# Optimization experiments

Measured on AMD Instinct MI355X. Metric: run time of the kernel, lower is better.

Reference implementation:

```python
import jax, jax.numpy as jnp
import numpy as np

N, M, DIM_K, DIM_V = 8192, 8192, 256, 256

def setup_inputs() -> dict:
    key = jax.random.key(0)
    kq, kk, kv = jax.random.split(key, 3)
    Q = jax.random.normal(kq, (N, DIM_K), dtype=jnp.float32)
    K = jax.random.normal(kk, (M, DIM_K), dtype=jnp.float32)
    V = jax.random.normal(kv, (M, DIM_V), dtype=jnp.float32)
    return {"Q": Q, "K": K, "V": V}

def reference(Q, K, V):
    # scores: [N, M] = Q @ K^T / sqrt(dim_k)
    scale = 1.0 / jnp.sqrt(jnp.asarray(Q.shape[-1], dtype=Q.dtype))
    scores = jnp.einsum('nd,md->nm', Q, K) * scale
    attn = jax.nn.softmax(scores, axis=-1)  # softmax over keys
    return attn @ V  # [N, dim_v]
```

## Files before the change

### kernel.cpp

```cpp
#include <hip/hip_runtime.h>
#include <hip/hip_bf16.h>


typedef __attribute__((ext_vector_type(16))) float floatx16;
typedef __attribute__((ext_vector_type(8)))  short short8;

union S8u { short8 v; unsigned short u[8]; };

__device__ __forceinline__ unsigned short f2bf(float f) {
    unsigned int u = __builtin_bit_cast(unsigned int, f);
    unsigned int r = u + 0x7fffu + ((u >> 16) & 1u);
    return (unsigned short)(r >> 16);
}

__device__ __forceinline__ unsigned cvtpk_bf16(float lo, float hi) {
    unsigned r;
    asm("v_cvt_pk_bf16_f32 %0, %1, %2" : "=v"(r) : "v"(lo), "v"(hi));
    return r;
}

__device__ __forceinline__ void gload16(const void* g, void* l) {
    __builtin_amdgcn_global_load_lds(
        (const __attribute__((address_space(1))) unsigned int*)g,
        (__attribute__((address_space(3))) unsigned int*)l, 16, 0, 0);
}


__global__ void cvt_bf16_kernel(const float* __restrict__ in,
                                unsigned short* __restrict__ out,
                                float scale, int n8) {
    int i = blockIdx.x * blockDim.x + threadIdx.x;
    if (i >= n8) return;
    const float4* p = reinterpret_cast<const float4*>(in) + (size_t)i * 2;
    float4 a = p[0], b = p[1];
    S8u r;
    r.u[0] = f2bf(a.x * scale); r.u[1] = f2bf(a.y * scale);
    r.u[2] = f2bf(a.z * scale); r.u[3] = f2bf(a.w * scale);
    r.u[4] = f2bf(b.x * scale); r.u[5] = f2bf(b.y * scale);
    r.u[6] = f2bf(b.z * scale); r.u[7] = f2bf(b.w * scale);
    *reinterpret_cast<short8*>(out + (size_t)i * 8) = r.v;
}

__global__ void transpose_v_kernel(const float* __restrict__ V,
                                   unsigned short* __restrict__ Vt) {
    __shared__ unsigned short T[64][72];
    const int kv0 = blockIdx.x * 64;
    const int v0  = blockIdx.y * 64;
    const int tid = threadIdx.x;
#pragma unroll
    for (int it = 0; it < 4; ++it) {
        int flat = it * 256 + tid;
        int r  = flat >> 4;
        int c4 = (flat & 15) * 4;
        float4 f = *reinterpret_cast<const float4*>(
            V + (size_t)(kv0 + r) * 256 + v0 + c4);
        T[c4 + 0][r] = f2bf(f.x);
        T[c4 + 1][r] = f2bf(f.y);
        T[c4 + 2][r] = f2bf(f.z);
        T[c4 + 3][r] = f2bf(f.w);
    }
    __syncthreads();
#pragma unroll
    for (int it = 0; it < 2; ++it) {
        int flat = it * 256 + tid;
        int r  = flat >> 3;
        int c8 = (flat & 7) * 8;
        short8 v8 = *reinterpret_cast<const short8*>(&T[r][c8]);
        *reinterpret_cast<short8*>(Vt + (size_t)(v0 + r) * 8192 + kv0 + c8) = v8;
    }
}


__global__ __launch_bounds__(512, 2)
void attn_kernel(const unsigned short* __restrict__ Qb,
                 const unsigned short* __restrict__ Kb,
                 const unsigned short* __restrict__ VtG,
                 float* __restrict__ Opart,
                 float* __restrict__ Ml,
                 int kv_span, int gshift) {
    __shared__ __align__(16) unsigned char lds[2][65536];

    const int tid  = threadIdx.x;
    const int lane = tid & 63;
    const int w    = tid >> 6;
    const int l31  = lane & 31;
    const int h    = lane >> 5;

    const int ngm1 = (1 << gshift) - 1;
    const int id   = blockIdx.x + 32 * blockIdx.y;
    const int g    = id & ngm1;
    const int qblk = id >> gshift;
    const int kv_begin = g * kv_span;
    const int tiles = kv_span >> 6;
    const int q0 = qblk * 256 + w * 32;

    short8 qf[16];
    {
        const unsigned short* qp = Qb + (size_t)(q0 + l31) * 256 + h * 8;
#pragma unroll
        for (int ds = 0; ds < 16; ++ds)
            qf[ds] = *reinterpret_cast<const short8*>(qp + ds * 16);
    }

    floatx16 o[8];
#pragma unroll
    for (int vt = 0; vt < 8; ++vt)
#pragma unroll
        for (int r = 0; r < 16; ++r) o[vt][r] = 0.f;
    float m_run = -1e30f, l_run = 0.f;

    auto STAGE = [&](int kv0, int bufsel) {
        unsigned char* kb = &lds[bufsel][0];
        unsigned char* vb = &lds[bufsel][32768];
#pragma unroll
        for (int i = 0; i < 4; ++i) {
            int j = w * 4 + i;
            {
                int row = j * 2 + (lane >> 5);
                int c   = lane & 31;
                int cs  = c ^ (row & 7);
                gload16(Kb + (size_t)(kv0 + row) * 256 + cs * 8, kb + j * 1024);
            }
            {
                int row = j * 8 + (lane >> 3);
                int c   = lane & 7;
                int cs  = c ^ (row & 7);
                gload16(VtG + (size_t)row * 8192 + kv0 + cs * 8, vb + j * 1024);
            }
        }
    };

    STAGE(kv_begin, 0);
    asm volatile("s_waitcnt vmcnt(0)" ::: "memory");
    __syncthreads();

    const int swz = l31 & 7;

    for (int t = 0; t < tiles; ++t) {
        const int cur = t & 1;
        if (t + 1 < tiles) STAGE(kv_begin + (t + 1) * 64, cur ^ 1);

        const unsigned char* kl = &lds[cur][0];
        const unsigned char* vl = &lds[cur][32768];

        floatx16 s0, s1;
#pragma unroll
        for (int r = 0; r < 16; ++r) { s0[r] = 0.f; s1[r] = 0.f; }
#pragma unroll
        for (int ds = 0; ds < 16; ++ds) {
            int c0 = (ds * 2 + h) ^ swz;
            short8 a0 = *reinterpret_cast<const short8*>(kl + (size_t)l31 * 512 + c0 * 16);
            short8 a1 = *reinterpret_cast<const short8*>(kl + (size_t)(l31 + 32) * 512 + c0 * 16);
            s0 = __builtin_amdgcn_mfma_f32_32x32x16_bf16(a0, qf[ds], s0, 0, 0, 0);
            s1 = __builtin_amdgcn_mfma_f32_32x32x16_bf16(a1, qf[ds], s1, 0, 0, 0);
        }

        float mt = s0[0];
#pragma unroll
        for (int r = 1; r < 16; ++r) mt = fmaxf(mt, s0[r]);
#pragma unroll
        for (int r = 0; r < 16; ++r) mt = fmaxf(mt, s1[r]);
        mt = fmaxf(mt, __shfl_xor(mt, 32));
        if (__any(mt > m_run + 8.0f)) {
            float mnew = fmaxf(m_run, mt);
            float al = __expf(m_run - mnew);
            m_run = mnew;
            l_run *= al;
#pragma unroll
            for (int reg = 0; reg < 16; ++reg) {
                int srcl = ((reg & 3) + 8 * (reg >> 2)) + 4 * h;
                float alr = __shfl(al, srcl);
#pragma unroll
                for (int vt = 0; vt < 8; ++vt) o[vt][reg] *= alr;
            }
        }
        float lt = 0.f;
#pragma unroll
        for (int r = 0; r < 16; ++r) { float p = __expf(s0[r] - m_run); s0[r] = p; lt += p; }
#pragma unroll
        for (int r = 0; r < 16; ++r) { float p = __expf(s1[r] - m_run); s1[r] = p; lt += p; }
        lt += __shfl_xor(lt, 32);
        l_run += lt;

        auto buildPA = [&](const floatx16& sv, int rbase) -> short8 {
            unsigned cpk0 = cvtpk_bf16(sv[rbase + 0], sv[rbase + 1]);
            unsigned cpk1 = cvtpk_bf16(sv[rbase + 2], sv[rbase + 3]);
            unsigned cpk2 = cvtpk_bf16(sv[rbase + 4], sv[rbase + 5]);
            unsigned cpk3 = cvtpk_bf16(sv[rbase + 6], sv[rbase + 7]);
            unsigned send0 = h ? cpk0 : cpk2;
            unsigned send1 = h ? cpk1 : cpk3;
            unsigned r0 = (unsigned)__shfl_xor((int)send0, 32);
            unsigned r1 = (unsigned)__shfl_xor((int)send1, 32);
            uint4 uu;
            uu.x = h ? r0 : cpk0;
            uu.y = h ? r1 : cpk1;
            uu.z = h ? cpk2 : r0;
            uu.w = h ? cpk3 : r1;
            return __builtin_bit_cast(short8, uu);
        };

#pragma unroll
        for (int kk = 0; kk < 4; ++kk) {
            short8 pa = buildPA((kk < 2) ? s0 : s1, (kk & 1) * 8);
            int cv = (kk * 2 + h) ^ swz;
#pragma unroll
            for (int vt = 0; vt < 8; ++vt) {
                short8 b = *reinterpret_cast<const short8*>(
                    vl + (size_t)(vt * 32 + l31) * 128 + cv * 16);
                o[vt] = __builtin_amdgcn_mfma_f32_32x32x16_bf16(pa, b, o[vt], 0, 0, 0);
            }
        }

        asm volatile("s_waitcnt vmcnt(0)" ::: "memory");
        __syncthreads();
    }

    const size_t gq = (size_t)g * 8192;
#pragma unroll
    for (int vt = 0; vt < 8; ++vt) {
#pragma unroll
        for (int reg = 0; reg < 16; ++reg) {
            int row = (reg & 3) + 8 * (reg >> 2) + 4 * h;
            Opart[(gq + q0 + row) * 256 + vt * 32 + l31] = o[vt][reg];
        }
    }
    if (h == 0) {
        size_t idx = (gq + q0 + l31) * 2;
        Ml[idx]     = m_run;
        Ml[idx + 1] = l_run;
    }
}


__global__ void merge_kernel(const float* __restrict__ Opart,
                             const float* __restrict__ Ml,
                             float* __restrict__ out, int ngroups) {
    int row = blockIdx.x;
    int col = threadIdx.x;
    float m = -1e30f;
    for (int g = 0; g < ngroups; ++g)
        m = fmaxf(m, Ml[((size_t)g * 8192 + row) * 2]);
    float den = 0.f, acc = 0.f;
    for (int g = 0; g < ngroups; ++g) {
        float wg = __expf(Ml[((size_t)g * 8192 + row) * 2] - m);
        den += wg * Ml[((size_t)g * 8192 + row) * 2 + 1];
        acc += wg * Opart[((size_t)g * 8192 + row) * 256 + col];
    }
    out[(size_t)row * 256 + col] = acc / den;
}


extern "C" void kernel_launch(void* const* d_in, const int* in_sizes, int n_in,
                              void* d_out, int out_size, void* d_ws, size_t ws_size,
                              hipStream_t stream) {
    const float* Q = (const float*)d_in[0];
    const float* K = (const float*)d_in[1];
    const float* V = (const float*)d_in[2];
    float* out = (float*)d_out;

    unsigned short* Qb = (unsigned short*)d_ws;
    unsigned short* Kb = Qb + (size_t)8192 * 256;
    unsigned short* Vt = Kb + (size_t)8192 * 256;

    const size_t base = (size_t)8192 * 256 * 2 * 3;
    const size_t osz  = (size_t)8192 * 256 * 4;
    const size_t mlsz = (size_t)8192 * 2 * 4;

    int gshift = 3;
    for (; gshift > 0; --gshift)
        if (base + ((osz + mlsz) << gshift) <= ws_size) break;

    int ng = 1 << gshift;
    float* Opart; float* Mlp;
    if (base + ((osz + mlsz) << gshift) <= ws_size) {
        Opart = (float*)((char*)d_ws + base);
        Mlp   = (float*)((char*)d_ws + base + osz * (size_t)ng);
    } else {
        gshift = 0; ng = 1;
        Opart = out;
        Mlp   = (float*)((char*)d_ws + base);
    }

    const int n8 = 8192 * 256 / 8;
    cvt_bf16_kernel<<<n8 / 256, 256, 0, stream>>>(Q, Qb, 0.0625f, n8);
    cvt_bf16_kernel<<<n8 / 256, 256, 0, stream>>>(K, Kb, 1.0f, n8);
    transpose_v_kernel<<<dim3(128, 4), 256, 0, stream>>>(V, Vt);
    attn_kernel<<<dim3(32, ng), 512, 0, stream>>>(Qb, Kb, Vt, Opart, Mlp,
                                                  8192 / ng, gshift);
    merge_kernel<<<8192, 256, 0, stream>>>(Opart, Mlp, out, ng);
}
```

Measured before the change: 142.9 us.

## Fuse Q conversion, use exp2 softmax, fp16 partials, setprio and permlane swap

Q is now converted to bf16 inside the attention kernel, with the scale folded in as log2(e)/16, which removes one conversion launch and its round trip through memory. The softmax uses exp2 and widens the rescale threshold. Partial outputs are normalized before being stored as fp16, which halves the partial buffer and the merge traffic. It also precomputes staging offsets, raises wave priority around the MFMA blocks, uses tree max/sum reductions, and uses permlane32_swap when available; the fp16 partials and larger threshold trade some precision and overflow headroom.

```diff
diff --git a/kernel.cpp b/kernel.cpp
--- a/kernel.cpp
+++ b/kernel.cpp
@@ -1,11 +1,18 @@
 #include <hip/hip_runtime.h>
 #include <hip/hip_bf16.h>
+#include <hip/hip_fp16.h>
 
 
 typedef __attribute__((ext_vector_type(16))) float floatx16;
 typedef __attribute__((ext_vector_type(8)))  short short8;
 
 union S8u { short8 v; unsigned short u[8]; };
+
+#if __has_builtin(__builtin_amdgcn_exp2f)
+#define EXP2F(x) __builtin_amdgcn_exp2f(x)
+#else
+#define EXP2F(x) exp2f(x)
+#endif
 
 __device__ __forceinline__ unsigned short f2bf(float f) {
     unsigned int u = __builtin_bit_cast(unsigned int, f);
@@ -72,10 +79,10 @@
 
 
 __global__ __launch_bounds__(512, 2)
-void attn_kernel(const unsigned short* __restrict__ Qb,
+void attn_kernel(const float* __restrict__ Qf,
                  const unsigned short* __restrict__ Kb,
                  const unsigned short* __restrict__ VtG,
-                 float* __restrict__ Opart,
+                 __half* __restrict__ Opart,
                  float* __restrict__ Ml,
                  int kv_span, int gshift) {
     __shared__ __align__(16) unsigned char lds[2][65536];
@@ -94,12 +101,21 @@
     const int tiles = kv_span >> 6;
     const int q0 = qblk * 256 + w * 32;
 
+    const float qs = 0.09016844005556021f;
     short8 qf[16];
     {
-        const unsigned short* qp = Qb + (size_t)(q0 + l31) * 256 + h * 8;
-#pragma unroll
-        for (int ds = 0; ds < 16; ++ds)
-            qf[ds] = *reinterpret_cast<const short8*>(qp + ds * 16);
+        const float* qp = Qf + (size_t)(q0 + l31) * 256 + h * 8;
+#pragma unroll
+        for (int ds = 0; ds < 16; ++ds) {
+            float4 f0 = *reinterpret_cast<const float4*>(qp + ds * 16);
+            float4 f1 = *reinterpret_cast<const float4*>(qp + ds * 16 + 4);
+            uint4 uu;
+            uu.x = cvtpk_bf16(f0.x * qs, f0.y * qs);
+            uu.y = cvtpk_bf16(f0.z * qs, f0.w * qs);
+            uu.z = cvtpk_bf16(f1.x * qs, f1.y * qs);
+            uu.w = cvtpk_bf16(f1.z * qs, f1.w * qs);
+            qf[ds] = __builtin_bit_cast(short8, uu);
+        }
     }
 
     floatx16 o[8];
@@ -108,25 +124,29 @@
 #pragma unroll
         for (int r = 0; r < 16; ++r) o[vt][r] = 0.f;
     float m_run = -1e30f, l_run = 0.f;
+
+    int offk[4], offv[4];
+#pragma unroll
+    for (int i = 0; i < 4; ++i) {
+        int j  = w * 4 + i;
+        int rk = j * 2 + (lane >> 5);
+        int ck = (lane & 31) ^ (rk & 7);
+        offk[i] = rk * 256 + ck * 8;
+        int rv = j * 8 + (lane >> 3);
+        int cv = (lane & 7) ^ (rv & 7);
+        offv[i] = rv * 8192 + cv * 8;
+    }
 
     auto STAGE = [&](int kv0, int bufsel) {
         unsigned char* kb = &lds[bufsel][0];
         unsigned char* vb = &lds[bufsel][32768];
+        const unsigned short* ks = Kb + (size_t)kv0 * 256;
+        const unsigned short* vs = VtG + kv0;
 #pragma unroll
         for (int i = 0; i < 4; ++i) {
             int j = w * 4 + i;
-            {
-                int row = j * 2 + (lane >> 5);
-                int c   = lane & 31;
-                int cs  = c ^ (row & 7);
-                gload16(Kb + (size_t)(kv0 + row) * 256 + cs * 8, kb + j * 1024);
-            }
-            {
-                int row = j * 8 + (lane >> 3);
-                int c   = lane & 7;
-                int cs  = c ^ (row & 7);
-                gload16(VtG + (size_t)row * 8192 + kv0 + cs * 8, vb + j * 1024);
-            }
+            gload16(ks + offk[i], kb + j * 1024);
+            gload16(vs + offv[i], vb + j * 1024);
         }
     };
 
@@ -146,6 +166,7 @@
         floatx16 s0, s1;
 #pragma unroll
         for (int r = 0; r < 16; ++r) { s0[r] = 0.f; s1[r] = 0.f; }
+        __builtin_amdgcn_s_setprio(1);
 #pragma unroll
         for (int ds = 0; ds < 16; ++ds) {
             int c0 = (ds * 2 + h) ^ swz;
@@ -154,16 +175,19 @@
             s0 = __builtin_amdgcn_mfma_f32_32x32x16_bf16(a0, qf[ds], s0, 0, 0, 0);
             s1 = __builtin_amdgcn_mfma_f32_32x32x16_bf16(a1, qf[ds], s1, 0, 0, 0);
         }
-
-        float mt = s0[0];
-#pragma unroll
-        for (int r = 1; r < 16; ++r) mt = fmaxf(mt, s0[r]);
-#pragma unroll
-        for (int r = 0; r < 16; ++r) mt = fmaxf(mt, s1[r]);
+        __builtin_amdgcn_s_setprio(0);
+
+        float t8[8];
+#pragma unroll
+        for (int i = 0; i < 8; ++i)
+            t8[i] = fmaxf(fmaxf(s0[i], s0[i + 8]), fmaxf(s1[i], s1[i + 8]));
+        float a0m = fmaxf(t8[0], t8[1]), a1m = fmaxf(t8[2], t8[3]);
+        float a2m = fmaxf(t8[4], t8[5]), a3m = fmaxf(t8[6], t8[7]);
+        float mt = fmaxf(fmaxf(a0m, a1m), fmaxf(a2m, a3m));
         mt = fmaxf(mt, __shfl_xor(mt, 32));
-        if (__any(mt > m_run + 8.0f)) {
+        if (__any(mt > m_run + 11.5f)) {
             float mnew = fmaxf(m_run, mt);
-            float al = __expf(m_run - mnew);
+            float al = EXP2F(m_run - mnew);
             m_run = mnew;
             l_run *= al;
 #pragma unroll
@@ -174,11 +198,15 @@
                 for (int vt = 0; vt < 8; ++vt) o[vt][reg] *= alr;
             }
         }
-        float lt = 0.f;
-#pragma unroll
-        for (int r = 0; r < 16; ++r) { float p = __expf(s0[r] - m_run); s0[r] = p; lt += p; }
-#pragma unroll
-        for (int r = 0; r < 16; ++r) { float p = __expf(s1[r] - m_run); s1[r] = p; lt += p; }
+#pragma unroll
+        for (int r = 0; r < 16; ++r) s0[r] = EXP2F(s0[r] - m_run);
+#pragma unroll
+        for (int r = 0; r < 16; ++r) s1[r] = EXP2F(s1[r] - m_run);
+        float u[8];
+#pragma unroll
+        for (int i = 0; i < 8; ++i)
+            u[i] = (s0[i] + s0[i + 8]) + (s1[i] + s1[i + 8]);
+        float lt = ((u[0] + u[1]) + (u[2] + u[3])) + ((u[4] + u[5]) + (u[6] + u[7]));
         lt += __shfl_xor(lt, 32);
         l_run += lt;
 
@@ -187,18 +215,26 @@
             unsigned cpk1 = cvtpk_bf16(sv[rbase + 2], sv[rbase + 3]);
             unsigned cpk2 = cvtpk_bf16(sv[rbase + 4], sv[rbase + 5]);
             unsigned cpk3 = cvtpk_bf16(sv[rbase + 6], sv[rbase + 7]);
+            uint4 uu;
+#if __has_builtin(__builtin_amdgcn_permlane32_swap)
+            auto r02 = __builtin_amdgcn_permlane32_swap((int)cpk0, (int)cpk2, false, false);
+            auto r13 = __builtin_amdgcn_permlane32_swap((int)cpk1, (int)cpk3, false, false);
+            uu.x = (unsigned)r02[0]; uu.y = (unsigned)r13[0];
+            uu.z = (unsigned)r02[1]; uu.w = (unsigned)r13[1];
+#else
             unsigned send0 = h ? cpk0 : cpk2;
             unsigned send1 = h ? cpk1 : cpk3;
             unsigned r0 = (unsigned)__shfl_xor((int)send0, 32);
             unsigned r1 = (unsigned)__shfl_xor((int)send1, 32);
-            uint4 uu;
             uu.x = h ? r0 : cpk0;
             uu.y = h ? r1 : cpk1;
             uu.z = h ? cpk2 : r0;
             uu.w = h ? cpk3 : r1;
+#endif
             return __builtin_bit_cast(short8, uu);
         };
 
+        __builtin_amdgcn_s_setprio(1);
 #pragma unroll
         for (int kk = 0; kk < 4; ++kk) {
             short8 pa = buildPA((kk < 2) ? s0 : s1, (kk & 1) * 8);
@@ -210,19 +246,22 @@
                 o[vt] = __builtin_amdgcn_mfma_f32_32x32x16_bf16(pa, b, o[vt], 0, 0, 0);
             }
         }
+        __builtin_amdgcn_s_setprio(0);
 
         asm volatile("s_waitcnt vmcnt(0)" ::: "memory");
         __syncthreads();
     }
 
     const size_t gq = (size_t)g * 8192;
-#pragma unroll
-    for (int vt = 0; vt < 8; ++vt) {
-#pragma unroll
-        for (int reg = 0; reg < 16; ++reg) {
-            int row = (reg & 3) + 8 * (reg >> 2) + 4 * h;
-            Opart[(gq + q0 + row) * 256 + vt * 32 + l31] = o[vt][reg];
-        }
+    float linv = 1.0f / l_run;
+#pragma unroll
+    for (int reg = 0; reg < 16; ++reg) {
+        int row = (reg & 3) + 8 * (reg >> 2) + 4 * h;
+        float li = __shfl(linv, row);
+#pragma unroll
+        for (int vt = 0; vt < 8; ++vt)
+            Opart[(gq + q0 + row) * 256 + vt * 32 + l31] =
+                __float2half_rn(o[vt][reg] * li);
     }
     if (h == 0) {
         size_t idx = (gq + q0 + l31) * 2;
@@ -232,7 +271,7 @@
 }
 
 
-__global__ void merge_kernel(const float* __restrict__ Opart,
+__global__ void merge_kernel(const __half* __restrict__ Opart,
                              const float* __restrict__ Ml,
                              float* __restrict__ out, int ngroups) {
     int row = blockIdx.x;
@@ -242,9 +281,10 @@
         m = fmaxf(m, Ml[((size_t)g * 8192 + row) * 2]);
     float den = 0.f, acc = 0.f;
     for (int g = 0; g < ngroups; ++g) {
-        float wg = __expf(Ml[((size_t)g * 8192 + row) * 2] - m);
-        den += wg * Ml[((size_t)g * 8192 + row) * 2 + 1];
-        acc += wg * Opart[((size_t)g * 8192 + row) * 256 + col];
+        float wg = EXP2F(Ml[((size_t)g * 8192 + row) * 2] - m) *
+                   Ml[((size_t)g * 8192 + row) * 2 + 1];
+        den += wg;
+        acc += wg * __half2float(Opart[((size_t)g * 8192 + row) * 256 + col]);
     }
     out[(size_t)row * 256 + col] = acc / den;
 }
@@ -258,34 +298,25 @@
     const float* V = (const float*)d_in[2];
     float* out = (float*)d_out;
 
-    unsigned short* Qb = (unsigned short*)d_ws;
-    unsigned short* Kb = Qb + (size_t)8192 * 256;
+    unsigned short* Kb = (unsigned short*)d_ws;
     unsigned short* Vt = Kb + (size_t)8192 * 256;
 
-    const size_t base = (size_t)8192 * 256 * 2 * 3;
-    const size_t osz  = (size_t)8192 * 256 * 4;
+    const size_t base = (size_t)8192 * 256 * 2 * 2;
+    const size_t osz  = (size_t)8192 * 256 * 2;
     const size_t mlsz = (size_t)8192 * 2 * 4;
 
     int gshift = 3;
     for (; gshift > 0; --gshift)
         if (base + ((osz + mlsz) << gshift) <= ws_size) break;
-
     int ng = 1 << gshift;
-    float* Opart; float* Mlp;
-    if (base + ((osz + mlsz) << gshift) <= ws_size) {
-        Opart = (float*)((char*)d_ws + base);
-        Mlp   = (float*)((char*)d_ws + base + osz * (size_t)ng);
-    } else {
-        gshift = 0; ng = 1;
-        Opart = out;
-        Mlp   = (float*)((char*)d_ws + base);
-    }
+
+    __half* Opart = (__half*)((char*)d_ws + base);
+    float*  Mlp   = (float*)((char*)d_ws + base + osz * (size_t)ng);
 
     const int n8 = 8192 * 256 / 8;
-    cvt_bf16_kernel<<<n8 / 256, 256, 0, stream>>>(Q, Qb, 0.0625f, n8);
     cvt_bf16_kernel<<<n8 / 256, 256, 0, stream>>>(K, Kb, 1.0f, n8);
     transpose_v_kernel<<<dim3(128, 4), 256, 0, stream>>>(V, Vt);
-    attn_kernel<<<dim3(32, ng), 512, 0, stream>>>(Qb, Kb, Vt, Opart, Mlp,
+    attn_kernel<<<dim3(32, ng), 512, 0, stream>>>(Q, Kb, Vt, Opart, Mlp,
                                                   8192 / ng, gshift);
     merge_kernel<<<8192, 256, 0, stream>>>(Opart, Mlp, out, ng);
 }
```

Result: faster. 137.1 us (-4.0%).
